# Performance work log

Measured on AMD Instinct MI355X. Metric: run time of the kernel, lower is better.

## Reference

```python
import jax, jax.numpy as jnp
import numpy as np

N = 100000
E = 1600000
F_IN, F_HID, F_OUT = 512, 512, 256
NEG_SLOPE = 0.01  # nn.LeakyReLU default


def setup_inputs() -> dict:
    key = jax.random.key(0)
    ks = jax.random.split(key, 16)
    def lin(k, fi, fo):
        s = 1.0 / np.sqrt(fi)
        return jax.random.uniform(k, (fi, fo), jnp.float32, -s, s)
    inp = {
        'x': jax.random.normal(ks[0], (N, F_IN), jnp.float32),
        'edge_index': jax.random.randint(ks[1], (2, E), 0, N, jnp.int64),
        'W1': lin(ks[2], F_IN, F_HID), 'b1': jnp.zeros((F_HID,), jnp.float32),
        'W2': lin(ks[3], F_HID, F_HID), 'b2': jnp.zeros((F_HID,), jnp.float32),
        'W3': lin(ks[4], F_HID, F_HID), 'b3': jnp.zeros((F_HID,), jnp.float32),
        'W4': lin(ks[5], F_HID, F_OUT), 'b4': jnp.zeros((F_OUT,), jnp.float32),
        'fcW1': lin(ks[6], F_OUT, 64), 'fcb1': jnp.zeros((64,), jnp.float32),
        'fcW2': lin(ks[7], 64, 1), 'fcb2': jnp.zeros((1,), jnp.float32),
    }
    return inp


def _gcn_norm(edge_index):
    # PyG gcn_norm with add_self_loops=True: deg counts incoming edges + 1 self loop
    src, dst = edge_index[0], edge_index[1]
    deg = jax.ops.segment_sum(jnp.ones((E,), jnp.float32), dst, num_segments=N) + 1.0
    dis = jax.lax.rsqrt(deg)  # deg >= 1 always (self loops)
    edge_norm = dis[src] * dis[dst]  # [E]
    self_norm = dis * dis            # [N], norm for the added self loop
    return src, dst, edge_norm, self_norm


def _gcn_layer(x, src, dst, edge_norm, self_norm, W, b):
    xw = x @ W  # transform-then-propagate (in < out not an issue here)
    agg = jax.ops.segment_sum(xw[src] * edge_norm[:, None], dst, num_segments=N)
    return agg + self_norm[:, None] * xw + b


def leaky(x):
    return jnp.where(x >= 0, x, NEG_SLOPE * x)


def reference(x, edge_index, W1, b1, W2, b2, W3, b3, W4, b4, fcW1, fcb1, fcW2, fcb2):
    src, dst, en, sn = _gcn_norm(edge_index)
    h = leaky(_gcn_layer(x, src, dst, en, sn, W1, b1))
    h = leaky(_gcn_layer(h, src, dst, en, sn, W2, b2))
    h = leaky(_gcn_layer(h, src, dst, en, sn, W3, b3))
    h = leaky(_gcn_layer(h, src, dst, en, sn, W4, b4))
    g = jnp.mean(h, axis=0, keepdims=True)  # global_mean_pool, batch=None -> [1, F_OUT]
    g = leaky(g @ fcW1 + fcb1)
    # dropout is identity in eval mode
    g = g @ fcW2 + fcb2
    return jax.nn.sigmoid(g)  # [1, 1]
```

## Files before the change

kernel.cpp:

```cpp
#include <hip/hip_runtime.h>
#include <hip/hip_bf16.h>
#include <cstdint>
#include <cstddef>


typedef unsigned short u16;
typedef unsigned char u8;
typedef unsigned int u32;
typedef __bf16 bf16x8 __attribute__((ext_vector_type(8)));
typedef u16 u16x8 __attribute__((ext_vector_type(8)));
typedef u32 u32x2 __attribute__((ext_vector_type(2)));
typedef float f32x2 __attribute__((ext_vector_type(2)));
typedef float f32x4 __attribute__((ext_vector_type(4)));

__device__ __forceinline__ u16 f2bf(float f) {
  u32 u = __builtin_bit_cast(u32, f);
  u += 0x7fffu + ((u >> 16) & 1u);
  return (u16)(u >> 16);
}
__device__ __forceinline__ float bf2f(u16 h) {
  return __builtin_bit_cast(float, (u32)h << 16);
}
__device__ __forceinline__ void g2lds16(const void* g, void* l) {
  __builtin_amdgcn_global_load_lds((__attribute__((address_space(1))) void*)g,
                                   (__attribute__((address_space(3))) void*)l, 16, 0, 0);
}

__global__ __launch_bounds__(256) void init_kernel(int* __restrict__ deg,
                                                   int* __restrict__ cursor,
                                                   float* __restrict__ pool, int N) {
  int i = blockIdx.x * 256 + threadIdx.x;
  if (i < N) { deg[i] = 0; cursor[i] = 0; }
  if (i < 256) pool[i] = 0.f;
}

__global__ void detect_kernel(const int* __restrict__ ei, int* __restrict__ flag) {
  __shared__ int nz;
  if (threadIdx.x == 0) nz = 0;
  __syncthreads();
  if (ei[2 * threadIdx.x + 1] != 0) atomicAdd(&nz, 1);
  __syncthreads();
  if (threadIdx.x == 0) *flag = (nz == 0) ? 1 : 0;
}

__device__ __forceinline__ int ld_src(const int* ei, int E, int e, int f64) {
  return f64 ? (int)((const long long*)ei)[e] : ei[e];
}
__device__ __forceinline__ int ld_dst(const int* ei, int E, int e, int f64) {
  return f64 ? (int)((const long long*)ei)[(long long)E + e] : ei[E + e];
}

__global__ __launch_bounds__(256) void degree_kernel(const int* __restrict__ ei,
                                                     const int* __restrict__ flag,
                                                     int* __restrict__ deg, int E) {
  int e = blockIdx.x * 256 + threadIdx.x;
  if (e >= E) return;
  int f = *flag;
  atomicAdd(&deg[ld_dst(ei, E, e, f)], 1);
}

__global__ __launch_bounds__(256) void dis_kernel(const int* __restrict__ deg,
                                                  float* __restrict__ dis, int N) {
  int i = blockIdx.x * 256 + threadIdx.x;
  if (i < N) dis[i] = rsqrtf((float)deg[i] + 1.0f);
}

__global__ __launch_bounds__(1024) void scan1_kernel(const int* __restrict__ deg,
                                                     int* __restrict__ rs,
                                                     int* __restrict__ bsum, int N) {
  __shared__ int s[1024];
  int tid = threadIdx.x;
  int i = blockIdx.x * 1024 + tid;
  int v = (i < N) ? deg[i] : 0;
  s[tid] = v;
  __syncthreads();
  for (int off = 1; off < 1024; off <<= 1) {
    int t = (tid >= off) ? s[tid - off] : 0;
    __syncthreads();
    s[tid] += t;
    __syncthreads();
  }
  if (i < N) rs[i] = s[tid] - v;
  if (tid == 1023) bsum[blockIdx.x] = s[1023];
}

__global__ void scan2_kernel(const int* __restrict__ bsum, int* __restrict__ boff, int nb) {
  if (threadIdx.x == 0) {
    int run = 0;
    for (int b = 0; b < nb; ++b) { boff[b] = run; run += bsum[b]; }
  }
}

__global__ __launch_bounds__(256) void scan3_kernel(int* __restrict__ rs,
                                                    const int* __restrict__ boff, int N) {
  int i = blockIdx.x * 256 + threadIdx.x;
  if (i < N) rs[i] += boff[i >> 10];
}

__global__ __launch_bounds__(256) void fill_kernel(const int* __restrict__ ei,
                                                   const int* __restrict__ flag,
                                                   const int* __restrict__ rs,
                                                   int* __restrict__ cursor,
                                                   int* __restrict__ colv, int E) {
  int e = blockIdx.x * 256 + threadIdx.x;
  if (e >= E) return;
  int f = *flag;
  int s = ld_src(ei, E, e, f);
  int d = ld_dst(ei, E, e, f);
  int p = atomicAdd(&cursor[d], 1);
  colv[rs[d] + p] = s;
}

__global__ __launch_bounds__(256) void convx_kernel(const float* __restrict__ x,
                                                    u16* __restrict__ xb, size_t n) {
  size_t i = ((size_t)blockIdx.x * 256 + threadIdx.x) * 4;
  if (i >= n) return;
  float4 v = *reinterpret_cast<const float4*>(x + i);
  typedef u16 u16x4 __attribute__((ext_vector_type(4)));
  u16x4 o;
  o[0] = f2bf(v.x); o[1] = f2bf(v.y); o[2] = f2bf(v.z); o[3] = f2bf(v.w);
  *reinterpret_cast<u16x4*>(xb + i) = o;
}

__global__ __launch_bounds__(256) void convw_kernel(const float* __restrict__ W,
                                                    u16* __restrict__ Wt, int Nout) {
  int id = blockIdx.x * 256 + threadIdx.x;
  if (id >= 512 * Nout) return;
  int k = id / Nout, n = id - k * Nout;
  Wt[n * 512 + k] = f2bf(W[id]);
}

template <bool OUT8, bool BACT>
__global__ __launch_bounds__(256, 2)
void gemm_kernel(const u16* __restrict__ A, const u16* __restrict__ Bt,
                 void* __restrict__ Cout, const float* __restrict__ bias,
                 int M, int Nout) {
  __shared__ u16 sA[128 * 32];
  __shared__ u16 sB[128 * 32];
  const int tid = threadIdx.x;
  const int wave = tid >> 6, lane = tid & 63;
  const int m0 = blockIdx.x * 128;
  const int n0 = blockIdx.y * 128;
  const int wm = (wave >> 1) * 64, wn = (wave & 1) * 64;
  const int lrow = lane >> 2, lchunk = lane & 3;
  const int fr = lane & 15, fq = (lane >> 4) * 8;

  f32x4 acc[4][4];
#pragma unroll
  for (int i = 0; i < 4; ++i)
#pragma unroll
    for (int j = 0; j < 4; ++j) acc[i][j] = (f32x4){0.f, 0.f, 0.f, 0.f};

  for (int k0 = 0; k0 < 512; k0 += 32) {
#pragma unroll
    for (int pss = 0; pss < 2; ++pss) {
      int rbase = pss * 64 + wave * 16;
      int arow = m0 + rbase + lrow;
      arow = arow < M ? arow : M - 1;
      g2lds16(A + (size_t)arow * 512 + k0 + lchunk * 8, &sA[rbase * 32]);
      int brow = n0 + rbase + lrow;
      g2lds16(Bt + (size_t)brow * 512 + k0 + lchunk * 8, &sB[rbase * 32]);
    }
    __builtin_amdgcn_s_waitcnt(0);
    __syncthreads();

    bf16x8 af[4], bfr[4];
#pragma unroll
    for (int t = 0; t < 4; ++t) {
      af[t]  = *reinterpret_cast<const bf16x8*>(&sA[(wm + t * 16 + fr) * 32 + fq]);
      bfr[t] = *reinterpret_cast<const bf16x8*>(&sB[(wn + t * 16 + fr) * 32 + fq]);
    }
#pragma unroll
    for (int i = 0; i < 4; ++i)
#pragma unroll
      for (int j = 0; j < 4; ++j)
        acc[i][j] = __builtin_amdgcn_mfma_f32_16x16x32_bf16(af[i], bfr[j], acc[i][j], 0, 0, 0);
    __syncthreads();
  }

  const int crow0 = m0 + wm + ((lane >> 4) << 2);
  const int ccol0 = n0 + wn + (lane & 15);
#pragma unroll
  for (int j = 0; j < 4; ++j) {
    const int col = ccol0 + j * 16;
    float bj = BACT ? bias[col] : 0.f;
#pragma unroll
    for (int i = 0; i < 4; ++i)
#pragma unroll
      for (int r = 0; r < 4; ++r) {
        int row = crow0 + i * 16 + r;
        if (row < M) {
          float v = acc[i][j][r];
          if (BACT) { v += bj; v = v >= 0.f ? v : 0.01f * v; }
          if (OUT8) {
            int e = __builtin_amdgcn_cvt_pk_fp8_f32(v, v, 0, false);
            ((u8*)Cout)[(size_t)row * Nout + col] = (u8)e;
          } else {
            ((u16*)Cout)[(size_t)row * Nout + col] = f2bf(v);
          }
        }
      }
  }
}

template <bool ACT, bool OUT8>
__global__ __launch_bounds__(256)
void agg_kernel(const u8* __restrict__ xw, const int* __restrict__ colv,
                const int* __restrict__ rs, const int* __restrict__ deg,
                const float* __restrict__ dis, const float* __restrict__ bias,
                void* __restrict__ hout, int N) {
  const int wave = threadIdx.x >> 6;
  const int lane = threadIdx.x & 63;
  const int node = blockIdx.x * 4 + wave;
  if (node >= N) return;
  const int start = rs[node];
  const int d = deg[node];
  const float dd = dis[node];
  const int fo = lane * 8;

  f32x2 acc[4];
#pragma unroll
  for (int i = 0; i < 4; ++i) acc[i] = (f32x2){0.f, 0.f};

  const int total = d + 1;
  for (int base = 0; base < total; base += 64) {
    int t = base + lane;
    int s = node;
    float w = 0.f;
    if (t < d)       { s = colv[start + t]; w = dd * dis[s]; }
    else if (t == d) { w = dd * dd; }
    int cnt = total - base;
    if (cnt > 64) cnt = 64;
    int cnt8 = (cnt + 7) & ~7;
    int wi = __builtin_bit_cast(int, w);
    for (int j = 0; j < cnt8; j += 8) {
      u32x2 v[8];
      float ws[8];
#pragma unroll
      for (int k = 0; k < 8; ++k) {
        int sk = __builtin_amdgcn_readlane(s, j + k);
        ws[k] = __builtin_bit_cast(float, __builtin_amdgcn_readlane(wi, j + k));
        v[k] = *reinterpret_cast<const u32x2*>(xw + (size_t)sk * 512 + fo);
      }
#pragma unroll
      for (int k = 0; k < 8; ++k) {
        f32x2 p0 = __builtin_amdgcn_cvt_pk_f32_fp8((int)v[k].x, false);
        f32x2 p1 = __builtin_amdgcn_cvt_pk_f32_fp8((int)v[k].x, true);
        f32x2 p2 = __builtin_amdgcn_cvt_pk_f32_fp8((int)v[k].y, false);
        f32x2 p3 = __builtin_amdgcn_cvt_pk_f32_fp8((int)v[k].y, true);
        f32x2 wv = (f32x2){ws[k], ws[k]};
        acc[0] += wv * p0;
        acc[1] += wv * p1;
        acc[2] += wv * p2;
        acc[3] += wv * p3;
      }
    }
  }

  float h[8];
#pragma unroll
  for (int i = 0; i < 8; ++i) {
    float v = (i & 1) ? acc[i >> 1].y : acc[i >> 1].x;
    if (ACT) { v += bias[fo + i]; v = v >= 0.f ? v : 0.01f * v; }
    h[i] = v;
  }
  if (OUT8) {
    int lo = __builtin_amdgcn_cvt_pk_fp8_f32(h[0], h[1], 0, false);
    lo = __builtin_amdgcn_cvt_pk_fp8_f32(h[2], h[3], lo, true);
    int hi = __builtin_amdgcn_cvt_pk_fp8_f32(h[4], h[5], 0, false);
    hi = __builtin_amdgcn_cvt_pk_fp8_f32(h[6], h[7], hi, true);
    u32x2 o; o.x = (u32)lo; o.y = (u32)hi;
    __builtin_nontemporal_store(o, reinterpret_cast<u32x2*>((u8*)hout + (size_t)node * 512 + fo));
  } else {
    u16x8 o;
#pragma unroll
    for (int i = 0; i < 8; ++i) o[i] = f2bf(h[i]);
    __builtin_nontemporal_store(o, reinterpret_cast<u16x8*>((u16*)hout + (size_t)node * 512 + fo));
  }
}

__global__ __launch_bounds__(256) void pool_kernel(const u16* __restrict__ h,
                                                   float* __restrict__ pool, int N) {
  __shared__ float lds[8 * 256];
  const int tid = threadIdx.x;
  const int fg = tid & 31;
  const int rg = tid >> 5;
  float acc[8];
#pragma unroll
  for (int i = 0; i < 8; ++i) acc[i] = 0.f;
  for (int r = blockIdx.x * 8 + rg; r < N; r += gridDim.x * 8) {
    u16x8 v = *reinterpret_cast<const u16x8*>(h + (size_t)r * 256 + fg * 8);
#pragma unroll
    for (int i = 0; i < 8; ++i) acc[i] += bf2f(v[i]);
  }
#pragma unroll
  for (int i = 0; i < 8; ++i) lds[rg * 256 + fg * 8 + i] = acc[i];
  __syncthreads();
  float s = 0.f;
#pragma unroll
  for (int g = 0; g < 8; ++g) s += lds[g * 256 + tid];
  atomicAdd(&pool[tid], s);
}

__global__ void fc_kernel(const float* __restrict__ pool, const float* __restrict__ fcW1,
                          const float* __restrict__ fcb1, const float* __restrict__ fcW2,
                          const float* __restrict__ fcb2, float* __restrict__ out,
                          float invN) {
  int j = threadIdx.x;
  float acc = 0.f;
  for (int f = 0; f < 256; ++f) acc += pool[f] * invN * fcW1[f * 64 + j];
  float h = acc + fcb1[j];
  h = h >= 0.f ? h : 0.01f * h;
  float p = h * fcW2[j];
  for (int o = 32; o; o >>= 1) p += __shfl_down(p, o);
  if (j == 0) out[0] = 1.f / (1.f + expf(-(p + fcb2[0])));
}

extern "C" void kernel_launch(void* const* d_in, const int* in_sizes, int n_in,
                              void* d_out, int out_size, void* d_ws, size_t ws_size,
                              hipStream_t stream) {
  const float* x    = (const float*)d_in[0];
  const int*   ei   = (const int*)d_in[1];
  const float* W1   = (const float*)d_in[2];
  const float* b1   = (const float*)d_in[3];
  const float* W2   = (const float*)d_in[4];
  const float* b2   = (const float*)d_in[5];
  const float* W3   = (const float*)d_in[6];
  const float* b3   = (const float*)d_in[7];
  const float* W4   = (const float*)d_in[8];
  const float* b4   = (const float*)d_in[9];
  const float* fcW1 = (const float*)d_in[10];
  const float* fcb1 = (const float*)d_in[11];
  const float* fcW2 = (const float*)d_in[12];
  const float* fcb2 = (const float*)d_in[13];
  float* out = (float*)d_out;

  const int N = in_sizes[0] / 512;
  const int E = in_sizes[1] / 2;

  char* p = (char*)d_ws;
  auto carve = [&](size_t bytes) {
    char* r = p;
    p += (bytes + 255) & ~(size_t)255;
    return r;
  };
  u16* bufX = (u16*)carve((size_t)N * 512 * 2);
  u16* bufH = (u16*)carve((size_t)N * 512 * 2);
  u8*  bufP = (u8*)carve((size_t)N * 512);
  u8*  bufQ = (u8*)carve((size_t)N * 512);
  u16* Wt1 = (u16*)carve(512 * 512 * 2);
  u16* Wt2 = (u16*)carve(512 * 512 * 2);
  u16* Wt3 = (u16*)carve(512 * 512 * 2);
  u16* Wt4 = (u16*)carve(512 * 256 * 2);
  int* deg    = (int*)carve((size_t)N * 4);
  int* cursor = (int*)carve((size_t)N * 4);
  int* rs     = (int*)carve((size_t)(N + 1) * 4);
  int* colv   = (int*)carve((size_t)E * 4);
  int* bsum   = (int*)carve(1024 * 4);
  int* boff   = (int*)carve(1024 * 4);
  int* flag   = (int*)carve(256);
  float* disv = (float*)carve((size_t)N * 4);
  float* pool = (float*)carve(256 * 4);
  if ((size_t)(p - (char*)d_ws) > ws_size) return;

  const int nb1024 = (N + 1023) / 1024;

  init_kernel<<<(N + 255) / 256, 256, 0, stream>>>(deg, cursor, pool, N);
  detect_kernel<<<1, 256, 0, stream>>>(ei, flag);
  degree_kernel<<<(E + 255) / 256, 256, 0, stream>>>(ei, flag, deg, E);
  dis_kernel<<<(N + 255) / 256, 256, 0, stream>>>(deg, disv, N);
  scan1_kernel<<<nb1024, 1024, 0, stream>>>(deg, rs, bsum, N);
  scan2_kernel<<<1, 64, 0, stream>>>(bsum, boff, nb1024);
  scan3_kernel<<<(N + 255) / 256, 256, 0, stream>>>(rs, boff, N);
  fill_kernel<<<(E + 255) / 256, 256, 0, stream>>>(ei, flag, rs, cursor, colv, E);

  convx_kernel<<<((size_t)N * 512 / 4 + 255) / 256, 256, 0, stream>>>(x, bufX, (size_t)N * 512);
  convw_kernel<<<(512 * 512 + 255) / 256, 256, 0, stream>>>(W1, Wt1, 512);
  convw_kernel<<<(512 * 512 + 255) / 256, 256, 0, stream>>>(W2, Wt2, 512);
  convw_kernel<<<(512 * 512 + 255) / 256, 256, 0, stream>>>(W3, Wt3, 512);
  convw_kernel<<<(512 * 256 + 255) / 256, 256, 0, stream>>>(W4, Wt4, 256);

  const unsigned gm = (unsigned)((N + 127) / 128);
  const unsigned ga = (unsigned)((N + 3) / 4);

  gemm_kernel<true, false><<<dim3(gm, 4), 256, 0, stream>>>(bufX, Wt1, bufP, nullptr, N, 512);
  agg_kernel<true, false><<<ga, 256, 0, stream>>>(bufP, colv, rs, deg, disv, b1, bufH, N);
  gemm_kernel<true, false><<<dim3(gm, 4), 256, 0, stream>>>(bufH, Wt2, bufP, nullptr, N, 512);
  agg_kernel<true, false><<<ga, 256, 0, stream>>>(bufP, colv, rs, deg, disv, b2, bufX, N);
  gemm_kernel<true, false><<<dim3(gm, 4), 256, 0, stream>>>(bufX, Wt3, bufP, nullptr, N, 512);
  agg_kernel<true, true><<<ga, 256, 0, stream>>>(bufP, colv, rs, deg, disv, b3, bufQ, N);
  agg_kernel<false, false><<<ga, 256, 0, stream>>>(bufQ, colv, rs, deg, disv, nullptr, bufH, N);
  gemm_kernel<false, true><<<dim3(gm, 2), 256, 0, stream>>>(bufH, Wt4, bufX, b4, N, 256);

  pool_kernel<<<256, 256, 0, stream>>>(bufX, pool, N);
  fc_kernel<<<1, 64, 0, stream>>>(pool, fcW1, fcb1, fcW2, fcb2, out, 1.0f / (float)N);
}
```

Measured before the change: 1.355 ms.

## Split aggregation across feature slices with edge-parallel lanes and shuffle reduction

The aggregation kernel now launches 8 feature slices per node group (2D grid). Within a wave, 8 lane groups each handle a different neighbor while 8 lanes cover a 64-byte slice, and a butterfly shuffle reduces the partial sums across groups. The aim is more parallelism for low-degree nodes and less serial readlane broadcasting per edge. In exchange, colv, dis and degree are read 8 times per node, each gather touches only a 64-byte segment of a source row, and the reduction adds shuffle overhead.

```diff
diff --git a/kernel.cpp b/kernel.cpp
--- a/kernel.cpp
+++ b/kernel.cpp
@@ -209,73 +209,76 @@
                 const int* __restrict__ rs, const int* __restrict__ deg,
                 const float* __restrict__ dis, const float* __restrict__ bias,
                 void* __restrict__ hout, int N) {
+  const int slice = blockIdx.x;
   const int wave = threadIdx.x >> 6;
   const int lane = threadIdx.x & 63;
-  const int node = blockIdx.x * 4 + wave;
+  const int node = blockIdx.y * 4 + wave;
   if (node >= N) return;
+  const int g = lane >> 3;
+  const int f = lane & 7;
   const int start = rs[node];
   const int d = deg[node];
   const float dd = dis[node];
-  const int fo = lane * 8;
+  const size_t fbyte = (size_t)slice * 64 + f * 8;
 
   f32x2 acc[4];
 #pragma unroll
   for (int i = 0; i < 4; ++i) acc[i] = (f32x2){0.f, 0.f};
 
   const int total = d + 1;
-  for (int base = 0; base < total; base += 64) {
-    int t = base + lane;
+  for (int base = 0; base < total; base += 8) {
+    int t = base + g;
     int s = node;
     float w = 0.f;
     if (t < d)       { s = colv[start + t]; w = dd * dis[s]; }
     else if (t == d) { w = dd * dd; }
-    int cnt = total - base;
-    if (cnt > 64) cnt = 64;
-    int cnt8 = (cnt + 7) & ~7;
-    int wi = __builtin_bit_cast(int, w);
-    for (int j = 0; j < cnt8; j += 8) {
-      u32x2 v[8];
-      float ws[8];
-#pragma unroll
-      for (int k = 0; k < 8; ++k) {
-        int sk = __builtin_amdgcn_readlane(s, j + k);
-        ws[k] = __builtin_bit_cast(float, __builtin_amdgcn_readlane(wi, j + k));
-        v[k] = *reinterpret_cast<const u32x2*>(xw + (size_t)sk * 512 + fo);
+    u32x2 v = *reinterpret_cast<const u32x2*>(xw + (size_t)s * 512 + fbyte);
+    f32x2 p0 = __builtin_amdgcn_cvt_pk_f32_fp8((int)v.x, false);
+    f32x2 p1 = __builtin_amdgcn_cvt_pk_f32_fp8((int)v.x, true);
+    f32x2 p2 = __builtin_amdgcn_cvt_pk_f32_fp8((int)v.y, false);
+    f32x2 p3 = __builtin_amdgcn_cvt_pk_f32_fp8((int)v.y, true);
+    f32x2 wv = (f32x2){w, w};
+    acc[0] += wv * p0;
+    acc[1] += wv * p1;
+    acc[2] += wv * p2;
+    acc[3] += wv * p3;
+  }
+
+#pragma unroll
+  for (int m = 8; m <= 32; m <<= 1) {
+#pragma unroll
+    for (int i = 0; i < 4; ++i) {
+      acc[i].x += __shfl_xor(acc[i].x, m);
+      acc[i].y += __shfl_xor(acc[i].y, m);
+    }
+  }
+
+  if (g == 0) {
+    float h[8];
+#pragma unroll
+    for (int i = 0; i < 8; ++i) {
+      float v = (i & 1) ? acc[i >> 1].y : acc[i >> 1].x;
+      if (ACT) {
+        v += bias[slice * 64 + f * 8 + i];
+        v = v >= 0.f ? v : 0.01f * v;
       }
-#pragma unroll
-      for (int k = 0; k < 8; ++k) {
-        f32x2 p0 = __builtin_amdgcn_cvt_pk_f32_fp8((int)v[k].x, false);
-        f32x2 p1 = __builtin_amdgcn_cvt_pk_f32_fp8((int)v[k].x, true);
-        f32x2 p2 = __builtin_amdgcn_cvt_pk_f32_fp8((int)v[k].y, false);
-        f32x2 p3 = __builtin_amdgcn_cvt_pk_f32_fp8((int)v[k].y, true);
-        f32x2 wv = (f32x2){ws[k], ws[k]};
-        acc[0] += wv * p0;
-        acc[1] += wv * p1;
-        acc[2] += wv * p2;
-        acc[3] += wv * p3;
-      }
+      h[i] = v;
     }
-  }
-
-  float h[8];
-#pragma unroll
-  for (int i = 0; i < 8; ++i) {
-    float v = (i & 1) ? acc[i >> 1].y : acc[i >> 1].x;
-    if (ACT) { v += bias[fo + i]; v = v >= 0.f ? v : 0.01f * v; }
-    h[i] = v;
-  }
-  if (OUT8) {
-    int lo = __builtin_amdgcn_cvt_pk_fp8_f32(h[0], h[1], 0, false);
-    lo = __builtin_amdgcn_cvt_pk_fp8_f32(h[2], h[3], lo, true);
-    int hi = __builtin_amdgcn_cvt_pk_fp8_f32(h[4], h[5], 0, false);
-    hi = __builtin_amdgcn_cvt_pk_fp8_f32(h[6], h[7], hi, true);
-    u32x2 o; o.x = (u32)lo; o.y = (u32)hi;
-    __builtin_nontemporal_store(o, reinterpret_cast<u32x2*>((u8*)hout + (size_t)node * 512 + fo));
-  } else {
-    u16x8 o;
-#pragma unroll
-    for (int i = 0; i < 8; ++i) o[i] = f2bf(h[i]);
-    __builtin_nontemporal_store(o, reinterpret_cast<u16x8*>((u16*)hout + (size_t)node * 512 + fo));
+    if (OUT8) {
+      int lo = __builtin_amdgcn_cvt_pk_fp8_f32(h[0], h[1], 0, false);
+      lo = __builtin_amdgcn_cvt_pk_fp8_f32(h[2], h[3], lo, true);
+      int hi = __builtin_amdgcn_cvt_pk_fp8_f32(h[4], h[5], 0, false);
+      hi = __builtin_amdgcn_cvt_pk_fp8_f32(h[6], h[7], hi, true);
+      u32x2 o; o.x = (u32)lo; o.y = (u32)hi;
+      __builtin_nontemporal_store(o,
+          reinterpret_cast<u32x2*>((u8*)hout + (size_t)node * 512 + fbyte));
+    } else {
+      u16x8 o;
+#pragma unroll
+      for (int i = 0; i < 8; ++i) o[i] = f2bf(h[i]);
+      __builtin_nontemporal_store(o,
+          reinterpret_cast<u16x8*>((u16*)hout + (size_t)node * 512 + slice * 64 + f * 8));
+    }
   }
 }
 
@@ -384,12 +387,12 @@
   const unsigned ga = (unsigned)((N + 3) / 4);
 
   gemm_kernel<true, false><<<dim3(gm, 4), 256, 0, stream>>>(bufX, Wt1, bufP, nullptr, N, 512);
-  agg_kernel<true, false><<<ga, 256, 0, stream>>>(bufP, colv, rs, deg, disv, b1, bufH, N);
+  agg_kernel<true, false><<<dim3(8, ga), 256, 0, stream>>>(bufP, colv, rs, deg, disv, b1, bufH, N);
   gemm_kernel<true, false><<<dim3(gm, 4), 256, 0, stream>>>(bufH, Wt2, bufP, nullptr, N, 512);
-  agg_kernel<true, false><<<ga, 256, 0, stream>>>(bufP, colv, rs, deg, disv, b2, bufX, N);
+  agg_kernel<true, false><<<dim3(8, ga), 256, 0, stream>>>(bufP, colv, rs, deg, disv, b2, bufX, N);
   gemm_kernel<true, false><<<dim3(gm, 4), 256, 0, stream>>>(bufX, Wt3, bufP, nullptr, N, 512);
-  agg_kernel<true, true><<<ga, 256, 0, stream>>>(bufP, colv, rs, deg, disv, b3, bufQ, N);
-  agg_kernel<false, false><<<ga, 256, 0, stream>>>(bufQ, colv, rs, deg, disv, nullptr, bufH, N);
+  agg_kernel<true, true><<<dim3(8, ga), 256, 0, stream>>>(bufP, colv, rs, deg, disv, b3, bufQ, N);
+  agg_kernel<false, false><<<dim3(8, ga), 256, 0, stream>>>(bufQ, colv, rs, deg, disv, nullptr, bufH, N);
   gemm_kernel<false, true><<<dim3(gm, 2), 256, 0, stream>>>(bufH, Wt4, bufX, b4, N, 256);
 
   pool_kernel<<<256, 256, 0, stream>>>(bufX, pool, N);
```

After: 2.579 ms. +90.3%, slower.

## Switch GEMM inputs and activations from bf16 to fp8 with fp8 MFMA

Applied to the files above, without the earlier changes.

Converts x, weights and all intermediate activations to fp8 (e4m3) and replaces the bf16 MFMA GEMM with an fp8 MFMA variant, halving the bytes of A/B operand traffic and the activation writes from aggregation. The GEMM's LDS staging is adapted to 1-byte elements, and the sequential single-thread block scan is replaced by a parallel LDS scan. This trades numerical precision for reduced memory traffic and higher MFMA throughput, which risks larger error against the reference.

```diff
diff --git a/kernel.cpp b/kernel.cpp
--- a/kernel.cpp
+++ b/kernel.cpp
@@ -7,7 +7,6 @@
 typedef unsigned short u16;
 typedef unsigned char u8;
 typedef unsigned int u32;
-typedef __bf16 bf16x8 __attribute__((ext_vector_type(8)));
 typedef u16 u16x8 __attribute__((ext_vector_type(8)));
 typedef u32 u32x2 __attribute__((ext_vector_type(2)));
 typedef float f32x2 __attribute__((ext_vector_type(2)));
@@ -84,11 +83,20 @@
   if (tid == 1023) bsum[blockIdx.x] = s[1023];
 }
 
-__global__ void scan2_kernel(const int* __restrict__ bsum, int* __restrict__ boff, int nb) {
-  if (threadIdx.x == 0) {
-    int run = 0;
-    for (int b = 0; b < nb; ++b) { boff[b] = run; run += bsum[b]; }
-  }
+__global__ __launch_bounds__(1024) void scan2_kernel(const int* __restrict__ bsum,
+                                                     int* __restrict__ boff, int nb) {
+  __shared__ int s[1024];
+  int tid = threadIdx.x;
+  int v = (tid < nb) ? bsum[tid] : 0;
+  s[tid] = v;
+  __syncthreads();
+  for (int off = 1; off < 1024; off <<= 1) {
+    int t = (tid >= off) ? s[tid - off] : 0;
+    __syncthreads();
+    s[tid] += t;
+    __syncthreads();
+  }
+  if (tid < nb) boff[tid] = s[tid] - v;
 }
 
 __global__ __launch_bounds__(256) void scan3_kernel(int* __restrict__ rs,
@@ -112,38 +120,40 @@
 }
 
 __global__ __launch_bounds__(256) void convx_kernel(const float* __restrict__ x,
-                                                    u16* __restrict__ xb, size_t n) {
+                                                    u8* __restrict__ x8, size_t n) {
   size_t i = ((size_t)blockIdx.x * 256 + threadIdx.x) * 4;
   if (i >= n) return;
   float4 v = *reinterpret_cast<const float4*>(x + i);
-  typedef u16 u16x4 __attribute__((ext_vector_type(4)));
-  u16x4 o;
-  o[0] = f2bf(v.x); o[1] = f2bf(v.y); o[2] = f2bf(v.z); o[3] = f2bf(v.w);
-  *reinterpret_cast<u16x4*>(xb + i) = o;
+  int lo = __builtin_amdgcn_cvt_pk_fp8_f32(v.x, v.y, 0, false);
+  int r = __builtin_amdgcn_cvt_pk_fp8_f32(v.z, v.w, lo, true);
+  *reinterpret_cast<u32*>(x8 + i) = (u32)r;
 }
 
 __global__ __launch_bounds__(256) void convw_kernel(const float* __restrict__ W,
-                                                    u16* __restrict__ Wt, int Nout) {
+                                                    u8* __restrict__ Wt, int Nout) {
   int id = blockIdx.x * 256 + threadIdx.x;
   if (id >= 512 * Nout) return;
   int k = id / Nout, n = id - k * Nout;
-  Wt[n * 512 + k] = f2bf(W[id]);
+  float v = W[id];
+  int e = __builtin_amdgcn_cvt_pk_fp8_f32(v, v, 0, false);
+  Wt[n * 512 + k] = (u8)e;
 }
 
 template <bool OUT8, bool BACT>
 __global__ __launch_bounds__(256, 2)
-void gemm_kernel(const u16* __restrict__ A, const u16* __restrict__ Bt,
-                 void* __restrict__ Cout, const float* __restrict__ bias,
-                 int M, int Nout) {
-  __shared__ u16 sA[128 * 32];
-  __shared__ u16 sB[128 * 32];
+void gemm8_kernel(const u8* __restrict__ A, const u8* __restrict__ Bt,
+                  void* __restrict__ Cout, const float* __restrict__ bias,
+                  int M, int Nout) {
+  __shared__ u8 sA[128 * 32];
+  __shared__ u8 sB[128 * 32];
   const int tid = threadIdx.x;
   const int wave = tid >> 6, lane = tid & 63;
   const int m0 = blockIdx.x * 128;
   const int n0 = blockIdx.y * 128;
   const int wm = (wave >> 1) * 64, wn = (wave & 1) * 64;
-  const int lrow = lane >> 2, lchunk = lane & 3;
-  const int fr = lane & 15, fq = (lane >> 4) * 8;
+  const int srow = wave * 32 + (lane >> 1);
+  const int soff = (lane & 1) * 16;
+  const int fr = lane & 15, fq8 = (lane >> 4) * 8;
 
   f32x4 acc[4][4];
 #pragma unroll
@@ -152,29 +162,27 @@
     for (int j = 0; j < 4; ++j) acc[i][j] = (f32x4){0.f, 0.f, 0.f, 0.f};
 
   for (int k0 = 0; k0 < 512; k0 += 32) {
-#pragma unroll
-    for (int pss = 0; pss < 2; ++pss) {
-      int rbase = pss * 64 + wave * 16;
-      int arow = m0 + rbase + lrow;
+    {
+      int arow = m0 + srow;
       arow = arow < M ? arow : M - 1;
-      g2lds16(A + (size_t)arow * 512 + k0 + lchunk * 8, &sA[rbase * 32]);
-      int brow = n0 + rbase + lrow;
-      g2lds16(Bt + (size_t)brow * 512 + k0 + lchunk * 8, &sB[rbase * 32]);
+      g2lds16(A + (size_t)arow * 512 + k0 + soff, &sA[(wave * 32) * 32]);
+      int brow = n0 + srow;
+      g2lds16(Bt + (size_t)brow * 512 + k0 + soff, &sB[(wave * 32) * 32]);
     }
     __builtin_amdgcn_s_waitcnt(0);
     __syncthreads();
 
-    bf16x8 af[4], bfr[4];
+    long long af[4], bf[4];
 #pragma unroll
     for (int t = 0; t < 4; ++t) {
-      af[t]  = *reinterpret_cast<const bf16x8*>(&sA[(wm + t * 16 + fr) * 32 + fq]);
-      bfr[t] = *reinterpret_cast<const bf16x8*>(&sB[(wn + t * 16 + fr) * 32 + fq]);
+      af[t] = *reinterpret_cast<const long long*>(&sA[(wm + t * 16 + fr) * 32 + fq8]);
+      bf[t] = *reinterpret_cast<const long long*>(&sB[(wn + t * 16 + fr) * 32 + fq8]);
     }
 #pragma unroll
     for (int i = 0; i < 4; ++i)
 #pragma unroll
       for (int j = 0; j < 4; ++j)
-        acc[i][j] = __builtin_amdgcn_mfma_f32_16x16x32_bf16(af[i], bfr[j], acc[i][j], 0, 0, 0);
+        acc[i][j] = __builtin_amdgcn_mfma_f32_16x16x32_fp8_fp8(af[i], bf[j], acc[i][j], 0, 0, 0);
     __syncthreads();
   }
 
@@ -203,12 +211,12 @@
   }
 }
 
-template <bool ACT, bool OUT8>
+template <bool ACT>
 __global__ __launch_bounds__(256)
 void agg_kernel(const u8* __restrict__ xw, const int* __restrict__ colv,
                 const int* __restrict__ rs, const int* __restrict__ deg,
                 const float* __restrict__ dis, const float* __restrict__ bias,
-                void* __restrict__ hout, int N) {
+                u8* __restrict__ hout, int N) {
   const int wave = threadIdx.x >> 6;
   const int lane = threadIdx.x & 63;
   const int node = blockIdx.x * 4 + wave;
@@ -264,19 +272,12 @@
     if (ACT) { v += bias[fo + i]; v = v >= 0.f ? v : 0.01f * v; }
     h[i] = v;
   }
-  if (OUT8) {
-    int lo = __builtin_amdgcn_cvt_pk_fp8_f32(h[0], h[1], 0, false);
-    lo = __builtin_amdgcn_cvt_pk_fp8_f32(h[2], h[3], lo, true);
-    int hi = __builtin_amdgcn_cvt_pk_fp8_f32(h[4], h[5], 0, false);
-    hi = __builtin_amdgcn_cvt_pk_fp8_f32(h[6], h[7], hi, true);
-    u32x2 o; o.x = (u32)lo; o.y = (u32)hi;
-    __builtin_nontemporal_store(o, reinterpret_cast<u32x2*>((u8*)hout + (size_t)node * 512 + fo));
-  } else {
-    u16x8 o;
-#pragma unroll
-    for (int i = 0; i < 8; ++i) o[i] = f2bf(h[i]);
-    __builtin_nontemporal_store(o, reinterpret_cast<u16x8*>((u16*)hout + (size_t)node * 512 + fo));
-  }
+  int lo = __builtin_amdgcn_cvt_pk_fp8_f32(h[0], h[1], 0, false);
+  lo = __builtin_amdgcn_cvt_pk_fp8_f32(h[2], h[3], lo, true);
+  int hi = __builtin_amdgcn_cvt_pk_fp8_f32(h[4], h[5], 0, false);
+  hi = __builtin_amdgcn_cvt_pk_fp8_f32(h[6], h[7], hi, true);
+  u32x2 o; o.x = (u32)lo; o.y = (u32)hi;
+  __builtin_nontemporal_store(o, reinterpret_cast<u32x2*>(hout + (size_t)node * 512 + fo));
 }
 
 __global__ __launch_bounds__(256) void pool_kernel(const u16* __restrict__ h,
@@ -344,14 +345,14 @@
     p += (bytes + 255) & ~(size_t)255;
     return r;
   };
-  u16* bufX = (u16*)carve((size_t)N * 512 * 2);
-  u16* bufH = (u16*)carve((size_t)N * 512 * 2);
+  u8*  bufX = (u8*)carve((size_t)N * 512);
   u8*  bufP = (u8*)carve((size_t)N * 512);
   u8*  bufQ = (u8*)carve((size_t)N * 512);
-  u16* Wt1 = (u16*)carve(512 * 512 * 2);
-  u16* Wt2 = (u16*)carve(512 * 512 * 2);
-  u16* Wt3 = (u16*)carve(512 * 512 * 2);
-  u16* Wt4 = (u16*)carve(512 * 256 * 2);
+  u16* bufH4 = (u16*)carve((size_t)N * 256 * 2);
+  u8* Wt1 = (u8*)carve(512 * 512);
+  u8* Wt2 = (u8*)carve(512 * 512);
+  u8* Wt3 = (u8*)carve(512 * 512);
+  u8* Wt4 = (u8*)carve(512 * 256);
   int* deg    = (int*)carve((size_t)N * 4);
   int* cursor = (int*)carve((size_t)N * 4);
   int* rs     = (int*)carve((size_t)(N + 1) * 4);
@@ -370,7 +371,7 @@
   degree_kernel<<<(E + 255) / 256, 256, 0, stream>>>(ei, flag, deg, E);
   dis_kernel<<<(N + 255) / 256, 256, 0, stream>>>(deg, disv, N);
   scan1_kernel<<<nb1024, 1024, 0, stream>>>(deg, rs, bsum, N);
-  scan2_kernel<<<1, 64, 0, stream>>>(bsum, boff, nb1024);
+  scan2_kernel<<<1, 1024, 0, stream>>>(bsum, boff, nb1024);
   scan3_kernel<<<(N + 255) / 256, 256, 0, stream>>>(rs, boff, N);
   fill_kernel<<<(E + 255) / 256, 256, 0, stream>>>(ei, flag, rs, cursor, colv, E);
 
@@ -383,15 +384,15 @@
   const unsigned gm = (unsigned)((N + 127) / 128);
   const unsigned ga = (unsigned)((N + 3) / 4);
 
-  gemm_kernel<true, false><<<dim3(gm, 4), 256, 0, stream>>>(bufX, Wt1, bufP, nullptr, N, 512);
-  agg_kernel<true, false><<<ga, 256, 0, stream>>>(bufP, colv, rs, deg, disv, b1, bufH, N);
-  gemm_kernel<true, false><<<dim3(gm, 4), 256, 0, stream>>>(bufH, Wt2, bufP, nullptr, N, 512);
-  agg_kernel<true, false><<<ga, 256, 0, stream>>>(bufP, colv, rs, deg, disv, b2, bufX, N);
-  gemm_kernel<true, false><<<dim3(gm, 4), 256, 0, stream>>>(bufX, Wt3, bufP, nullptr, N, 512);
-  agg_kernel<true, true><<<ga, 256, 0, stream>>>(bufP, colv, rs, deg, disv, b3, bufQ, N);
-  agg_kernel<false, false><<<ga, 256, 0, stream>>>(bufQ, colv, rs, deg, disv, nullptr, bufH, N);
-  gemm_kernel<false, true><<<dim3(gm, 2), 256, 0, stream>>>(bufH, Wt4, bufX, b4, N, 256);
-
-  pool_kernel<<<256, 256, 0, stream>>>(bufX, pool, N);
+  gemm8_kernel<true, false><<<dim3(gm, 4), 256, 0, stream>>>(bufX, Wt1, bufP, nullptr, N, 512);
+  agg_kernel<true><<<ga, 256, 0, stream>>>(bufP, colv, rs, deg, disv, b1, bufQ, N);
+  gemm8_kernel<true, false><<<dim3(gm, 4), 256, 0, stream>>>(bufQ, Wt2, bufP, nullptr, N, 512);
+  agg_kernel<true><<<ga, 256, 0, stream>>>(bufP, colv, rs, deg, disv, b2, bufX, N);
+  gemm8_kernel<true, false><<<dim3(gm, 4), 256, 0, stream>>>(bufX, Wt3, bufP, nullptr, N, 512);
+  agg_kernel<true><<<ga, 256, 0, stream>>>(bufP, colv, rs, deg, disv, b3, bufQ, N);
+  agg_kernel<false><<<ga, 256, 0, stream>>>(bufQ, colv, rs, deg, disv, nullptr, bufX, N);
+  gemm8_kernel<false, true><<<dim3(gm, 2), 256, 0, stream>>>(bufX, Wt4, bufH4, b4, N, 256);
+
+  pool_kernel<<<256, 256, 0, stream>>>(bufH4, pool, N);
   fc_kernel<<<1, 64, 0, stream>>>(pool, fcW1, fcb1, fcW2, fcb2, out, 1.0f / (float)N);
 }
```

Result: faster. 1.276 ms (-5.8%).
